# Kernel optimization log

Measured on AMD Instinct MI355X. Metric: run time of the kernel, lower is better.

Reference implementation:

```python
import jax, jax.numpy as jnp
import numpy as np

BETA = 0.25  # commitment/codebook mixing as in VQVAE.__init__


def setup_inputs() -> dict:
    key = jax.random.key(0)
    k1, k2 = jax.random.split(key)
    # z: encoder latent [B, C, H, W] with C = latent_dim
    z = jax.random.normal(k1, (32, 64, 64, 64), dtype=jnp.float32)
    # codebook: nn.Embedding(num_embeddings, latent_dim).weight
    codebook = jax.random.normal(k2, (1024, 64), dtype=jnp.float32)
    return {"z": z, "codebook": codebook}


def reference(z, codebook):
    B, C, H, W = z.shape
    zf = z.reshape(B, C, H * W).transpose(0, 2, 1)  # [B, N, C], N = H*W
    # Squared Euclidean distances; argmin identical to torch.cdist(p=2) argmin
    # since sqrt is monotone (min_distances are unused in the original forward).
    d2 = (jnp.sum(zf * zf, axis=-1, keepdims=True)              # [B, N, 1]
          + jnp.sum(codebook * codebook, axis=-1)[None, None, :]  # [1, 1, K]
          - 2.0 * jnp.einsum('bnc,kc->bnk', zf, codebook))        # [B, N, K]
    indices = jnp.argmin(d2, axis=-1)                            # [B, N]
    z_q = codebook[indices]                                      # [B, N, C] gather
    z_q = z_q.transpose(0, 2, 1).reshape(B, C, H, W)
    commitment_loss = jnp.mean((jax.lax.stop_gradient(z_q) - z) ** 2)
    codebook_loss = jnp.mean((z_q - jax.lax.stop_gradient(z)) ** 2)
    loss = commitment_loss + BETA * codebook_loss
    return z_q, loss
```

## Files before the change

### kernel.cpp

```cpp
#include <hip/hip_runtime.h>
#include <float.h>

#define HW    4096
#define NC    64
#define NK    1024
#define NB    32
#define NPIX  (NB*HW)
#define TOTAL (NPIX*NC)
#define PPB   256

#define MARGIN 8e-3f

typedef __attribute__((ext_vector_type(8))) short short8;
typedef __attribute__((ext_vector_type(4))) float floatx4;

__device__ __forceinline__ unsigned short f2bf(float f) {
    unsigned u = __float_as_uint(f);
    u += 0x7FFFu + ((u >> 16) & 1u);
    return (unsigned short)(u >> 16);
}
__device__ __forceinline__ float bf2f(unsigned short h) {
    return __uint_as_float(((unsigned)h) << 16);
}

__device__ __forceinline__ void ins3f(float& b1, int& i1, float& b2, int& i2,
                                      float& b3, float s, int k) {
    bool lt1 = s < b1;
    bool lt2 = s < b2;
    bool lt3 = s < b3;
    b3 = lt2 ? b2 : (lt3 ? s : b3);
    b2 = lt1 ? b1 : (lt2 ? s : b2);
    i2 = lt1 ? i1 : (lt2 ? k : i2);
    b1 = lt1 ? s : b1;
    i1 = lt1 ? k : i1;
}
__device__ __forceinline__ void ins3t(float& b1, int& i1, float& b2, int& i2,
                                      float& b3, float s, int k) {
    bool lt1 = (s < b1) || (s == b1 && k < i1);
    bool lt2 = (s < b2) || (s == b2 && k < i2);
    bool lt3 = s < b3;
    b3 = lt2 ? b2 : (lt3 ? s : b3);
    b2 = lt1 ? b1 : (lt2 ? s : b2);
    i2 = lt1 ? i1 : (lt2 ? k : i2);
    b1 = lt1 ? s : b1;
    i1 = lt1 ? k : i1;
}

__global__ void vq_prep_kernel(const float* __restrict__ cb,
                               float* __restrict__ cnorm,
                               unsigned short* __restrict__ cb_hi,
                               unsigned short* __restrict__ cb_lo,
                               float* __restrict__ loss_out) {
    int k = blockIdx.x * 256 + threadIdx.x;
    if (k == 0) loss_out[0] = 0.0f;
    if (k < NK) {
        double s = 0.0;
        #pragma unroll 4
        for (int c = 0; c < NC; ++c) {
            float f = cb[k * NC + c];
            unsigned short h = f2bf(f);
            unsigned short l = f2bf(f - bf2f(h));
            cb_hi[k * NC + c] = h;
            cb_lo[k * NC + c] = l;
            double v = (double)f;
            s = fma(v, v, s);
        }
        cnorm[k] = (float)s;
    }
}

__global__ __launch_bounds__(256, 2) void vq_mfma_kernel(
        const float* __restrict__ z,
        const float* __restrict__ cb,
        const unsigned short* __restrict__ cb_hi,
        const unsigned short* __restrict__ cb_lo,
        const float* __restrict__ cnorm,
        float* __restrict__ zq,
        float* __restrict__ loss_out) {
    __shared__ unsigned short zh[64][PPB];
    __shared__ unsigned short zl[64][PPB];
    __shared__ alignas(16) float cn_lds[NK];
    __shared__ float rb1[PPB], rb2[PPB], rb3[PPB];
    __shared__ int   ri1[PPB], ri2[PPB];
    __shared__ int   finidx[PPB];
    __shared__ int   flags[PPB];
    __shared__ float redf[4];

    const int tid = threadIdx.x;
    const int g0  = blockIdx.x * PPB;
    const int bb  = g0 >> 12;
    const int pp0 = g0 & 4095;
    const float* zbase = z  + (size_t)bb * (NC * HW) + pp0;
    float*      zqbase = zq + (size_t)bb * (NC * HW) + pp0;

    ((float4*)cn_lds)[tid] = ((const float4*)cnorm)[tid];

    {
        const int px4 = (tid & 63) * 4;
        const int c0  = tid >> 6;
        #pragma unroll
        for (int it = 0; it < 16; ++it) {
            const int c = it * 4 + c0;
            float4 v = *(const float4*)(zbase + (size_t)c * HW + px4);
            unsigned short h0 = f2bf(v.x), h1 = f2bf(v.y),
                           h2 = f2bf(v.z), h3 = f2bf(v.w);
            unsigned short l0 = f2bf(v.x - bf2f(h0)), l1 = f2bf(v.y - bf2f(h1)),
                           l2 = f2bf(v.z - bf2f(h2)), l3 = f2bf(v.w - bf2f(h3));
            uint2 ph = make_uint2((unsigned)h0 | ((unsigned)h1 << 16),
                                  (unsigned)h2 | ((unsigned)h3 << 16));
            uint2 pl = make_uint2((unsigned)l0 | ((unsigned)l1 << 16),
                                  (unsigned)l2 | ((unsigned)l3 << 16));
            *(uint2*)&zh[c][px4] = ph;
            *(uint2*)&zl[c][px4] = pl;
        }
    }
    __syncthreads();

    const int lane = tid & 63;
    const int w    = tid >> 6;
    const int q    = lane >> 4;
    const int pcol = lane & 15;

    short8 Bh0[4], Bh1[4], Bl0[4], Bl1[4];
    #pragma unroll
    for (int j = 0; j < 4; ++j) {
        const int px = w * 64 + j * 16 + pcol;
        #pragma unroll
        for (int t = 0; t < 8; ++t) {
            Bh0[j][t] = (short)zh[q * 8 + t][px];
            Bh1[j][t] = (short)zh[32 + q * 8 + t][px];
            Bl0[j][t] = (short)zl[q * 8 + t][px];
            Bl1[j][t] = (short)zl[32 + q * 8 + t][px];
        }
    }

    const short8* cbh8 = (const short8*)cb_hi;
    const short8* cbl8 = (const short8*)cb_lo;

    float B1[4], B2[4], B3[4];
    int   I1[4], I2[4];
    #pragma unroll
    for (int j = 0; j < 4; ++j) {
        B1[j] = FLT_MAX; B2[j] = FLT_MAX; B3[j] = FLT_MAX;
        I1[j] = 0; I2[j] = 0;
    }

    short8 nah0 = cbh8[pcol * 8 + q];
    short8 nah1 = cbh8[pcol * 8 + 4 + q];
    short8 nal0 = cbl8[pcol * 8 + q];
    short8 nal1 = cbl8[pcol * 8 + 4 + q];

    #pragma unroll 2
    for (int tile = 0; tile < 64; ++tile) {
        short8 ah0 = nah0, ah1 = nah1, al0 = nal0, al1 = nal1;
        if (tile < 63) {
            const int r = (tile + 1) * 16 + pcol;
            nah0 = cbh8[r * 8 + q];
            nah1 = cbh8[r * 8 + 4 + q];
            nal0 = cbl8[r * 8 + q];
            nal1 = cbl8[r * 8 + 4 + q];
        }
        const float4 cn4 = *(const float4*)&cn_lds[tile * 16 + q * 4];
        const int kb = tile * 16 + q * 4;
        #pragma unroll
        for (int j = 0; j < 4; ++j) {
            floatx4 a0 = {0.f, 0.f, 0.f, 0.f};
            floatx4 a1 = {0.f, 0.f, 0.f, 0.f};
            a0 = __builtin_amdgcn_mfma_f32_16x16x32_bf16(ah0, Bh0[j], a0, 0, 0, 0);
            a1 = __builtin_amdgcn_mfma_f32_16x16x32_bf16(ah1, Bh1[j], a1, 0, 0, 0);
            a0 = __builtin_amdgcn_mfma_f32_16x16x32_bf16(ah0, Bl0[j], a0, 0, 0, 0);
            a1 = __builtin_amdgcn_mfma_f32_16x16x32_bf16(ah1, Bl1[j], a1, 0, 0, 0);
            a0 = __builtin_amdgcn_mfma_f32_16x16x32_bf16(al0, Bh0[j], a0, 0, 0, 0);
            a1 = __builtin_amdgcn_mfma_f32_16x16x32_bf16(al1, Bh1[j], a1, 0, 0, 0);

            float s0 = fmaf(-2.f, a0[0] + a1[0], cn4.x);
            float s1 = fmaf(-2.f, a0[1] + a1[1], cn4.y);
            float s2 = fmaf(-2.f, a0[2] + a1[2], cn4.z);
            float s3 = fmaf(-2.f, a0[3] + a1[3], cn4.w);
            ins3f(B1[j], I1[j], B2[j], I2[j], B3[j], s0, kb + 0);
            ins3f(B1[j], I1[j], B2[j], I2[j], B3[j], s1, kb + 1);
            ins3f(B1[j], I1[j], B2[j], I2[j], B3[j], s2, kb + 2);
            ins3f(B1[j], I1[j], B2[j], I2[j], B3[j], s3, kb + 3);
        }
    }

    #pragma unroll
    for (int j = 0; j < 4; ++j) {
        float b1v = B1[j], b2v = B2[j], b3v = B3[j];
        int i1 = I1[j], i2 = I2[j];
        #pragma unroll
        for (int d = 16; d <= 32; d <<= 1) {
            float ob1 = __shfl_xor(b1v, d);
            int   oi1 = __shfl_xor(i1, d);
            float ob2 = __shfl_xor(b2v, d);
            int   oi2 = __shfl_xor(i2, d);
            float ob3 = __shfl_xor(b3v, d);
            ins3t(b1v, i1, b2v, i2, b3v, ob1, oi1);
            ins3t(b1v, i1, b2v, i2, b3v, ob2, oi2);
            b3v = fminf(b3v, ob3);
        }
        if (q == 0) {
            const int px = w * 64 + j * 16 + pcol;
            rb1[px] = b1v; rb2[px] = b2v; rb3[px] = b3v;
            ri1[px] = i1;  ri2[px] = i2;
        }
    }
    __syncthreads();

    int flag = 0;
    {
        const int p = tid;
        int fi = ri1[p];
        const float g3 = rb3[p] - rb1[p];
        const float g2 = rb2[p] - rb1[p];
        if (g3 < MARGIN) {
            flag = 1;
        } else if (g2 < MARGIN) {
            const float* zp = zbase + p;
            const int ia = fi, ib = ri2[p];
            const float* ra  = cb + (size_t)ia * NC;
            const float* rbp = cb + (size_t)ib * NC;
            double sa = 0.0, sb = 0.0;
            for (int c = 0; c < NC; ++c) {
                double zv = (double)zp[(size_t)c * HW];
                double ta = zv - (double)ra[c];
                double tb = zv - (double)rbp[c];
                sa = fma(ta, ta, sa);
                sb = fma(tb, tb, sb);
            }
            if (sb < sa || (sb == sa && ib < ia)) fi = ib;
        }
        finidx[p] = fi;
        flags[p]  = flag;
    }
    const int nflag = __syncthreads_count(flag);

    if (nflag > 0) {
        double* red_s = reinterpret_cast<double*>(cn_lds);
        int*    red_i = reinterpret_cast<int*>(cn_lds + 512);
        for (int p = 0; p < PPB; ++p) {
            if (flags[p]) {
                const float* zp = zbase + p;
                double bd = 1.0e300; int bi = 0;
                #pragma unroll 1
                for (int r = 0; r < 4; ++r) {
                    const int k = tid * 4 + r;
                    const float* rowp = cb + (size_t)k * NC;
                    double s = 0.0;
                    for (int c = 0; c < NC; ++c) {
                        double t = (double)zp[(size_t)c * HW] - (double)rowp[c];
                        s = fma(t, t, s);
                    }
                    if (s < bd) { bd = s; bi = k; }
                }
                red_s[tid] = bd; red_i[tid] = bi;
                __syncthreads();
                if (tid < 64) {
                    double m = red_s[tid]; int mi = red_i[tid];
                    #pragma unroll
                    for (int t = 1; t < 4; ++t) {
                        double om = red_s[tid + 64 * t];
                        int    oi = red_i[tid + 64 * t];
                        if (om < m || (om == m && oi < mi)) { m = om; mi = oi; }
                    }
                    #pragma unroll
                    for (int off = 32; off > 0; off >>= 1) {
                        double om = __shfl_down(m, off);
                        int    oi = __shfl_down(mi, off);
                        if (om < m || (om == m && oi < mi)) { m = om; mi = oi; }
                    }
                    if (tid == 0) finidx[p] = mi;
                }
                __syncthreads();
            }
        }
        __syncthreads();
    }

    {
        const int p  = tid;
        const int fi = finidx[p];
        const float4* crow4 = (const float4*)(cb + (size_t)fi * NC);
        float sse = 0.f;
        #pragma unroll
        for (int j = 0; j < 16; ++j) {
            const float4 qv = crow4[j];
            const size_t c0 = (size_t)(4 * j) * HW + p;
            const float z0 = zbase[c0];
            const float z1 = zbase[c0 + HW];
            const float z2 = zbase[c0 + 2 * (size_t)HW];
            const float z3 = zbase[c0 + 3 * (size_t)HW];
            zqbase[c0]                  = qv.x;
            zqbase[c0 + HW]             = qv.y;
            zqbase[c0 + 2 * (size_t)HW] = qv.z;
            zqbase[c0 + 3 * (size_t)HW] = qv.w;
            float t0 = qv.x - z0, t1 = qv.y - z1, t2 = qv.z - z2, t3 = qv.w - z3;
            sse = fmaf(t0, t0, sse);
            sse = fmaf(t1, t1, sse);
            sse = fmaf(t2, t2, sse);
            sse = fmaf(t3, t3, sse);
        }
        #pragma unroll
        for (int off = 32; off > 0; off >>= 1) sse += __shfl_down(sse, off);
        if ((tid & 63) == 0) redf[tid >> 6] = sse;
        __syncthreads();
        if (tid == 0)
            atomicAdd(loss_out, (redf[0] + redf[1] + redf[2] + redf[3]) *
                                (1.25f / (float)TOTAL));
    }
}

extern "C" void kernel_launch(void* const* d_in, const int* in_sizes, int n_in,
                              void* d_out, int out_size, void* d_ws, size_t ws_size,
                              hipStream_t stream) {
    const float* z  = (const float*)d_in[0];
    const float* cb = (const float*)d_in[1];
    float* out      = (float*)d_out;
    float* zqp      = out;
    float* loss     = out + TOTAL;

    float* cnorm          = (float*)d_ws;
    unsigned short* cb_hi = (unsigned short*)((char*)d_ws + 4096);
    unsigned short* cb_lo = (unsigned short*)((char*)d_ws + 4096 + NK * NC * 2);

    vq_prep_kernel<<<4, 256, 0, stream>>>(cb, cnorm, cb_hi, cb_lo, loss);
    vq_mfma_kernel<<<NPIX / PPB, 256, 0, stream>>>(z, cb, cb_hi, cb_lo, cnorm,
                                                   zqp, loss);
}
```

Measured before the change: 197.4 us.

## Halve pixels per block, raise occupancy, use med3 top-3 insert, vectorize prep

Halves the pixels per block from 256 to 128, so each wave keeps 2 pixel tiles of B fragments and top-3 state instead of 4, and raises the launch bound to 4 blocks per CU to improve latency hiding. The codebook tile prefetch register double-buffer is removed, and the top-3 insertion now uses fmed3/fmin to cut select instructions. The prep kernel reads codebook rows as float4 and launches 16x64 threads. The epilogue splits each pixel's 64 channels across two thread halves. In exchange, each block does less MFMA work per codebook fragment load, so codebook traffic from L2 doubles and the inner loop loses its explicit prefetch.

```diff
diff --git a/kernel.cpp b/kernel.cpp
--- a/kernel.cpp
+++ b/kernel.cpp
@@ -7,7 +7,7 @@
 #define NB    32
 #define NPIX  (NB*HW)
 #define TOTAL (NPIX*NC)
-#define PPB   256
+#define PPB   128
 
 #define MARGIN 8e-3f
 
@@ -26,24 +26,26 @@
 __device__ __forceinline__ void ins3f(float& b1, int& i1, float& b2, int& i2,
                                       float& b3, float s, int k) {
     bool lt1 = s < b1;
-    bool lt2 = s < b2;
-    bool lt3 = s < b3;
-    b3 = lt2 ? b2 : (lt3 ? s : b3);
-    b2 = lt1 ? b1 : (lt2 ? s : b2);
+    bool lt2 = s <= b2;
+    float nb3 = __builtin_amdgcn_fmed3f(s, b2, b3);
+    float nb2 = __builtin_amdgcn_fmed3f(s, b1, b2);
     i2 = lt1 ? i1 : (lt2 ? k : i2);
-    b1 = lt1 ? s : b1;
     i1 = lt1 ? k : i1;
+    b1 = fminf(s, b1);
+    b2 = nb2;
+    b3 = nb3;
 }
 __device__ __forceinline__ void ins3t(float& b1, int& i1, float& b2, int& i2,
                                       float& b3, float s, int k) {
     bool lt1 = (s < b1) || (s == b1 && k < i1);
     bool lt2 = (s < b2) || (s == b2 && k < i2);
-    bool lt3 = s < b3;
-    b3 = lt2 ? b2 : (lt3 ? s : b3);
-    b2 = lt1 ? b1 : (lt2 ? s : b2);
+    float nb3 = __builtin_amdgcn_fmed3f(s, b2, b3);
+    float nb2 = lt1 ? b1 : (lt2 ? s : b2);
     i2 = lt1 ? i1 : (lt2 ? k : i2);
+    i1 = lt1 ? k : i1;
     b1 = lt1 ? s : b1;
-    i1 = lt1 ? k : i1;
+    b2 = nb2;
+    b3 = nb3;
 }
 
 __global__ void vq_prep_kernel(const float* __restrict__ cb,
@@ -51,25 +53,31 @@
                                unsigned short* __restrict__ cb_hi,
                                unsigned short* __restrict__ cb_lo,
                                float* __restrict__ loss_out) {
-    int k = blockIdx.x * 256 + threadIdx.x;
+    int k = blockIdx.x * 64 + threadIdx.x;
     if (k == 0) loss_out[0] = 0.0f;
     if (k < NK) {
+        const float4* r4 = (const float4*)(cb + (size_t)k * NC);
         double s = 0.0;
-        #pragma unroll 4
-        for (int c = 0; c < NC; ++c) {
-            float f = cb[k * NC + c];
-            unsigned short h = f2bf(f);
-            unsigned short l = f2bf(f - bf2f(h));
-            cb_hi[k * NC + c] = h;
-            cb_lo[k * NC + c] = l;
-            double v = (double)f;
-            s = fma(v, v, s);
+        #pragma unroll
+        for (int j = 0; j < 16; ++j) {
+            float4 v = r4[j];
+            const float fv[4] = {v.x, v.y, v.z, v.w};
+            #pragma unroll
+            for (int t = 0; t < 4; ++t) {
+                float f = fv[t];
+                unsigned short h = f2bf(f);
+                unsigned short l = f2bf(f - bf2f(h));
+                cb_hi[k * NC + 4 * j + t] = h;
+                cb_lo[k * NC + 4 * j + t] = l;
+                double dv = (double)f;
+                s = fma(dv, dv, s);
+            }
         }
         cnorm[k] = (float)s;
     }
 }
 
-__global__ __launch_bounds__(256, 2) void vq_mfma_kernel(
+__global__ __launch_bounds__(256, 4) void vq_mfma_kernel(
         const float* __restrict__ z,
         const float* __restrict__ cb,
         const unsigned short* __restrict__ cb_hi,
@@ -96,11 +104,11 @@
     ((float4*)cn_lds)[tid] = ((const float4*)cnorm)[tid];
 
     {
-        const int px4 = (tid & 63) * 4;
-        const int c0  = tid >> 6;
-        #pragma unroll
-        for (int it = 0; it < 16; ++it) {
-            const int c = it * 4 + c0;
+        const int px4 = (tid & 31) * 4;
+        const int c0  = tid >> 5;
+        #pragma unroll
+        for (int it = 0; it < 8; ++it) {
+            const int c = it * 8 + c0;
             float4 v = *(const float4*)(zbase + (size_t)c * HW + px4);
             unsigned short h0 = f2bf(v.x), h1 = f2bf(v.y),
                            h2 = f2bf(v.z), h3 = f2bf(v.w);
@@ -121,10 +129,10 @@
     const int q    = lane >> 4;
     const int pcol = lane & 15;
 
-    short8 Bh0[4], Bh1[4], Bl0[4], Bl1[4];
+    short8 Bh0[2], Bh1[2], Bl0[2], Bl1[2];
     #pragma unroll
-    for (int j = 0; j < 4; ++j) {
-        const int px = w * 64 + j * 16 + pcol;
+    for (int j = 0; j < 2; ++j) {
+        const int px = w * 32 + j * 16 + pcol;
         #pragma unroll
         for (int t = 0; t < 8; ++t) {
             Bh0[j][t] = (short)zh[q * 8 + t][px];
@@ -137,33 +145,26 @@
     const short8* cbh8 = (const short8*)cb_hi;
     const short8* cbl8 = (const short8*)cb_lo;
 
-    float B1[4], B2[4], B3[4];
-    int   I1[4], I2[4];
+    float B1[2], B2[2], B3[2];
+    int   I1[2], I2[2];
     #pragma unroll
-    for (int j = 0; j < 4; ++j) {
+    for (int j = 0; j < 2; ++j) {
         B1[j] = FLT_MAX; B2[j] = FLT_MAX; B3[j] = FLT_MAX;
         I1[j] = 0; I2[j] = 0;
     }
 
-    short8 nah0 = cbh8[pcol * 8 + q];
-    short8 nah1 = cbh8[pcol * 8 + 4 + q];
-    short8 nal0 = cbl8[pcol * 8 + q];
-    short8 nal1 = cbl8[pcol * 8 + 4 + q];
-
     #pragma unroll 2
     for (int tile = 0; tile < 64; ++tile) {
-        short8 ah0 = nah0, ah1 = nah1, al0 = nal0, al1 = nal1;
-        if (tile < 63) {
-            const int r = (tile + 1) * 16 + pcol;
-            nah0 = cbh8[r * 8 + q];
-            nah1 = cbh8[r * 8 + 4 + q];
-            nal0 = cbl8[r * 8 + q];
-            nal1 = cbl8[r * 8 + 4 + q];
-        }
+        const int r = tile * 16 + pcol;
+        short8 ah0 = cbh8[r * 8 + q];
+        short8 ah1 = cbh8[r * 8 + 4 + q];
+        short8 al0 = cbl8[r * 8 + q];
+        short8 al1 = cbl8[r * 8 + 4 + q];
+
         const float4 cn4 = *(const float4*)&cn_lds[tile * 16 + q * 4];
         const int kb = tile * 16 + q * 4;
         #pragma unroll
-        for (int j = 0; j < 4; ++j) {
+        for (int j = 0; j < 2; ++j) {
             floatx4 a0 = {0.f, 0.f, 0.f, 0.f};
             floatx4 a1 = {0.f, 0.f, 0.f, 0.f};
             a0 = __builtin_amdgcn_mfma_f32_16x16x32_bf16(ah0, Bh0[j], a0, 0, 0, 0);
@@ -185,7 +186,7 @@
     }
 
     #pragma unroll
-    for (int j = 0; j < 4; ++j) {
+    for (int j = 0; j < 2; ++j) {
         float b1v = B1[j], b2v = B2[j], b3v = B3[j];
         int i1 = I1[j], i2 = I2[j];
         #pragma unroll
@@ -200,7 +201,7 @@
             b3v = fminf(b3v, ob3);
         }
         if (q == 0) {
-            const int px = w * 64 + j * 16 + pcol;
+            const int px = w * 32 + j * 16 + pcol;
             rb1[px] = b1v; rb2[px] = b2v; rb3[px] = b3v;
             ri1[px] = i1;  ri2[px] = i2;
         }
@@ -208,7 +209,7 @@
     __syncthreads();
 
     int flag = 0;
-    {
+    if (tid < PPB) {
         const int p = tid;
         int fi = ri1[p];
         const float g3 = rb3[p] - rb1[p];
@@ -278,14 +279,15 @@
     }
 
     {
-        const int p  = tid;
+        const int p  = tid & (PPB - 1);
+        const int qq = tid >> 7;
         const int fi = finidx[p];
-        const float4* crow4 = (const float4*)(cb + (size_t)fi * NC);
+        const float4* crow4 = (const float4*)(cb + (size_t)fi * NC) + qq * 8;
         float sse = 0.f;
         #pragma unroll
-        for (int j = 0; j < 16; ++j) {
+        for (int j = 0; j < 8; ++j) {
             const float4 qv = crow4[j];
-            const size_t c0 = (size_t)(4 * j) * HW + p;
+            const size_t c0 = (size_t)(qq * 32 + 4 * j) * HW + p;
             const float z0 = zbase[c0];
             const float z1 = zbase[c0 + HW];
             const float z2 = zbase[c0 + 2 * (size_t)HW];
@@ -323,7 +325,7 @@
     unsigned short* cb_hi = (unsigned short*)((char*)d_ws + 4096);
     unsigned short* cb_lo = (unsigned short*)((char*)d_ws + 4096 + NK * NC * 2);
 
-    vq_prep_kernel<<<4, 256, 0, stream>>>(cb, cnorm, cb_hi, cb_lo, loss);
+    vq_prep_kernel<<<16, 64, 0, stream>>>(cb, cnorm, cb_hi, cb_lo, loss);
     vq_mfma_kernel<<<NPIX / PPB, 256, 0, stream>>>(z, cb, cb_hi, cb_lo, cnorm,
                                                    zqp, loss);
 }
```

After: 225.6 us. 14.3% more time.
